# Kernel optimization log

Hardware: AMD Instinct MI355X
Metric: run time of the kernel (lower is better)

Reference implementation:

```python
import jax, jax.numpy as jnp
import numpy as np
from math import sqrt

B, N, D = 16, 4096, 128
M = 64 * 24  # mem_size_per_joint * num_joints


def setup_inputs() -> dict:
    key = jax.random.key(0)
    kx, km = jax.random.split(key)
    x = jax.random.normal(kx, (B, N, D), dtype=jnp.float32)
    mem = jax.random.normal(km, (1, D, M), dtype=jnp.float32)  # N(0,1) init as in torch
    return {"x": x, "mem": mem}


def reference(x, mem):
    # x: (B, N, D); mem: (1, D, M)
    d = x.shape[-1]
    w = mem[0]  # (D, M)
    # logits = bmm(m_key (B,M,D), x_ (B,D,N)) / sqrt(D)  -> (B, M, N)
    logits = jnp.einsum('dm,bnd->bmn', w, x) / sqrt(d)
    # softmax over the memory axis (dim=1 in torch layout)
    attn = jax.nn.softmax(logits, axis=1)  # (B, M, N)
    # x_new = bmm(m (B,D,M), attn) -> (B,D,N); output permuted to (B,N,D)
    out = jnp.einsum('dm,bmn->bnd', w, attn)
    return out
```

## Files before the change

### kernel.cpp

```cpp
#include <hip/hip_runtime.h>
#include <math.h>


#define Bdim 16
#define Ndim 4096
#define Ddim 128
#define Mdim 1536
#define NT 64
#define NTHREADS 256
#define NSESS 12
#define SESS_M 128
#define XPAD 136
#define PPAD 136
#define NFRAG 24576

typedef __attribute__((ext_vector_type(8))) _Float16 f16x8;
typedef __attribute__((ext_vector_type(4))) _Float16 f16x4;
typedef __attribute__((ext_vector_type(4))) float    f32x4;

__global__ void jamb_prep(const float* __restrict__ w,
                          _Float16* __restrict__ wt,
                          _Float16* __restrict__ wd) {
    const int tid = blockIdx.x * 256 + threadIdx.x;
    const float SC = 0.08838834764831843f;
    if (tid < NFRAG) {
        const int f    = tid;
        const int lane = f & 63;
        const int fs   = f >> 6;
        const int ks   = fs & 3;
        const int mt   = fs >> 2;
        const int m    = mt * 16 + (lane & 15);
        const int d0   = ks * 32 + (lane >> 4) * 8;
        f16x8 pk;
        #pragma unroll
        for (int j = 0; j < 8; ++j)
            pk[j] = (_Float16)(w[(size_t)(d0 + j) * Mdim + m] * SC);
        *(f16x8*)&wt[(size_t)f * 8] = pk;
    } else {
        const int f    = tid - NFRAG;
        const int lane = f & 63;
        const int fs   = f >> 6;
        const int km   = fs % 48;
        const int dt   = fs / 48;
        const int d    = dt * 16 + (lane & 15);
        const int m0   = km * 32 + (lane >> 4) * 8;
        const float* src = w + (size_t)d * Mdim + m0;
        const float4 v0 = *(const float4*)src;
        const float4 v1 = *(const float4*)(src + 4);
        f16x8 pk;
        pk[0] = (_Float16)v0.x; pk[1] = (_Float16)v0.y;
        pk[2] = (_Float16)v0.z; pk[3] = (_Float16)v0.w;
        pk[4] = (_Float16)v1.x; pk[5] = (_Float16)v1.y;
        pk[6] = (_Float16)v1.z; pk[7] = (_Float16)v1.w;
        *(f16x8*)&wd[(size_t)f * 8] = pk;
    }
}

__global__ __launch_bounds__(NTHREADS, 4)
void jamb_mfma_kernel(const float* __restrict__ x,
                      const _Float16* __restrict__ wt,
                      const _Float16* __restrict__ wd,
                      float* __restrict__ out) {
    __shared__ __align__(16) _Float16 xs[NT * XPAD];
    __shared__ __align__(16) _Float16 Pbuf[NT * PPAD];
    __shared__ float redsum[4][4][16];

    const int t    = threadIdx.x;
    const int w    = t >> 6;
    const int l    = t & 63;
    const int c16  = l & 15;
    const int quad = l >> 4;

    const int blk   = blockIdx.x;
    const int b     = blk >> 6;
    const int nbase = (blk & 63) * NT;

    {
        const float* xb = x + (size_t)(b * Ndim + nbase) * Ddim;
        #pragma unroll
        for (int i = 0; i < 8; ++i) {
            const int f   = t + i * 256;
            const int row = f >> 5;
            const int c4  = (f & 31) * 4;
            const float4 v = *(const float4*)(xb + row * Ddim + c4);
            f16x4 pk;
            pk[0] = (_Float16)v.x; pk[1] = (_Float16)v.y;
            pk[2] = (_Float16)v.z; pk[3] = (_Float16)v.w;
            *(f16x4*)&xs[row * XPAD + c4] = pk;
        }
    }
    __syncthreads();

    const f16x8* WT = (const f16x8*)wt;
    const f16x8* WD = (const f16x8*)wd;

    float sums[4] = {0.f, 0.f, 0.f, 0.f};
    f32x4 c[2][4];
    #pragma unroll
    for (int i = 0; i < 2; ++i)
        #pragma unroll
        for (int nt = 0; nt < 4; ++nt) c[i][nt] = (f32x4){0.f, 0.f, 0.f, 0.f};

    #pragma unroll 1
    for (int q = 0; q < NSESS; ++q) {
        const int mtb = q * 8 + w * 2;

        f32x4 acc[2][4];
        #pragma unroll
        for (int i = 0; i < 2; ++i)
            #pragma unroll
            for (int nt = 0; nt < 4; ++nt) acc[i][nt] = (f32x4){0.f, 0.f, 0.f, 0.f};

        #pragma unroll
        for (int s = 0; s < 4; ++s) {
            const f16x8 fh0 = WT[((mtb + 0) * 4 + s) * 64 + l];
            const f16x8 fh1 = WT[((mtb + 1) * 4 + s) * 64 + l];
            f16x8 bx[4];
            #pragma unroll
            for (int nt = 0; nt < 4; ++nt)
                bx[nt] = *(const f16x8*)&xs[(nt * 16 + c16) * XPAD + s * 32 + quad * 8];
            #pragma unroll
            for (int nt = 0; nt < 4; ++nt) {
                acc[0][nt] = __builtin_amdgcn_mfma_f32_16x16x32_f16(fh0, bx[nt], acc[0][nt], 0, 0, 0);
                acc[1][nt] = __builtin_amdgcn_mfma_f32_16x16x32_f16(fh1, bx[nt], acc[1][nt], 0, 0, 0);
            }
        }

        #pragma unroll
        for (int i = 0; i < 2; ++i) {
            const int mloc = (w * 2 + i) * 16 + quad * 4;
            #pragma unroll
            for (int nt = 0; nt < 4; ++nt) {
                const float e0 = __expf(acc[i][nt][0]);
                const float e1 = __expf(acc[i][nt][1]);
                const float e2 = __expf(acc[i][nt][2]);
                const float e3 = __expf(acc[i][nt][3]);
                sums[nt] += (e0 + e1) + (e2 + e3);
                f16x4 pk;
                pk[0] = (_Float16)e0; pk[1] = (_Float16)e1;
                pk[2] = (_Float16)e2; pk[3] = (_Float16)e3;
                *(f16x4*)&Pbuf[(nt * 16 + c16) * PPAD + mloc] = pk;
            }
        }
        __syncthreads();

        #pragma unroll
        for (int sk = 0; sk < 4; ++sk) {
            const f16x8 a0 = WD[((2 * w)     * 48 + q * 4 + sk) * 64 + l];
            const f16x8 a1 = WD[((2 * w + 1) * 48 + q * 4 + sk) * 64 + l];
            f16x8 p[4];
            #pragma unroll
            for (int nt = 0; nt < 4; ++nt)
                p[nt] = *(const f16x8*)&Pbuf[(nt * 16 + c16) * PPAD + sk * 32 + quad * 8];
            #pragma unroll
            for (int nt = 0; nt < 4; ++nt) {
                c[0][nt] = __builtin_amdgcn_mfma_f32_16x16x32_f16(a0, p[nt], c[0][nt], 0, 0, 0);
                c[1][nt] = __builtin_amdgcn_mfma_f32_16x16x32_f16(a1, p[nt], c[1][nt], 0, 0, 0);
            }
        }
        __syncthreads();
    }

    #pragma unroll
    for (int nt = 0; nt < 4; ++nt) {
        sums[nt] += __shfl_xor(sums[nt], 16, 64);
        sums[nt] += __shfl_xor(sums[nt], 32, 64);
    }
    if (quad == 0) {
        #pragma unroll
        for (int nt = 0; nt < 4; ++nt) redsum[w][nt][c16] = sums[nt];
    }
    __syncthreads();

    float inv[4];
    #pragma unroll
    for (int nt = 0; nt < 4; ++nt)
        inv[nt] = 1.f / ((redsum[0][nt][c16] + redsum[1][nt][c16]) +
                         (redsum[2][nt][c16] + redsum[3][nt][c16]));

    #pragma unroll
    for (int dt2 = 0; dt2 < 2; ++dt2) {
        #pragma unroll
        for (int nt = 0; nt < 4; ++nt) {
            float* op = out + (size_t)(b * Ndim + nbase + nt * 16 + c16) * Ddim
                           + (2 * w + dt2) * 16 + quad * 4;
            float4 o;
            o.x = c[dt2][nt][0] * inv[nt];
            o.y = c[dt2][nt][1] * inv[nt];
            o.z = c[dt2][nt][2] * inv[nt];
            o.w = c[dt2][nt][3] * inv[nt];
            *(float4*)op = o;
        }
    }
}

extern "C" void kernel_launch(void* const* d_in, const int* in_sizes, int n_in,
                              void* d_out, int out_size, void* d_ws, size_t ws_size,
                              hipStream_t stream) {
    const float* x = (const float*)d_in[0];
    const float* w = (const float*)d_in[1];
    float* out = (float*)d_out;
    (void)in_sizes; (void)n_in; (void)out_size; (void)ws_size;

    _Float16* wt = (_Float16*)d_ws;
    _Float16* wd = wt + Ddim * Mdim;

    jamb_prep<<<dim3((2 * NFRAG) / 256), dim3(256), 0, stream>>>(w, wt, wd);
    jamb_mfma_kernel<<<dim3((Bdim * Ndim) / NT), dim3(NTHREADS), 0, stream>>>(x, wt, wd, out);
}
```

Baseline: 132.6 us.

## Double-buffer softmax tile and overlap logits with output MFMA in smaller sessions

```diff
diff --git a/kernel.cpp b/kernel.cpp
--- a/kernel.cpp
+++ b/kernel.cpp
@@ -8,10 +8,10 @@
 #define Mdim 1536
 #define NT 64
 #define NTHREADS 256
-#define NSESS 12
-#define SESS_M 128
+#define NSESS 24
+#define SESS_M 64
 #define XPAD 136
-#define PPAD 136
+#define PPAD 72
 #define NFRAG 24576
 
 typedef __attribute__((ext_vector_type(8))) _Float16 f16x8;
@@ -22,7 +22,7 @@
                           _Float16* __restrict__ wt,
                           _Float16* __restrict__ wd) {
     const int tid = blockIdx.x * 256 + threadIdx.x;
-    const float SC = 0.08838834764831843f;
+    const float SC = 0.12751742957f;
     if (tid < NFRAG) {
         const int f    = tid;
         const int lane = f & 63;
@@ -62,7 +62,7 @@
                       const _Float16* __restrict__ wd,
                       float* __restrict__ out) {
     __shared__ __align__(16) _Float16 xs[NT * XPAD];
-    __shared__ __align__(16) _Float16 Pbuf[NT * PPAD];
+    __shared__ __align__(16) _Float16 Pbuf[2][NT * PPAD];
     __shared__ float redsum[4][4][16];
 
     const int t    = threadIdx.x;
@@ -101,65 +101,74 @@
         #pragma unroll
         for (int nt = 0; nt < 4; ++nt) c[i][nt] = (f32x4){0.f, 0.f, 0.f, 0.f};
 
-    #pragma unroll 1
-    for (int q = 0; q < NSESS; ++q) {
-        const int mtb = q * 8 + w * 2;
-
-        f32x4 acc[2][4];
-        #pragma unroll
-        for (int i = 0; i < 2; ++i)
-            #pragma unroll
-            for (int nt = 0; nt < 4; ++nt) acc[i][nt] = (f32x4){0.f, 0.f, 0.f, 0.f};
-
+    f16x8 fh[4];
+
+    auto p1load = [&](int sess) {
+        const int mt = sess * 4 + w;
+        #pragma unroll
+        for (int s = 0; s < 4; ++s)
+            fh[s] = WT[(mt * 4 + s) * 64 + l];
+    };
+
+    auto p1 = [&](int sess) {
+        f32x4 acc[4];
+        #pragma unroll
+        for (int nt = 0; nt < 4; ++nt) acc[nt] = (f32x4){0.f, 0.f, 0.f, 0.f};
         #pragma unroll
         for (int s = 0; s < 4; ++s) {
-            const f16x8 fh0 = WT[((mtb + 0) * 4 + s) * 64 + l];
-            const f16x8 fh1 = WT[((mtb + 1) * 4 + s) * 64 + l];
             f16x8 bx[4];
             #pragma unroll
             for (int nt = 0; nt < 4; ++nt)
                 bx[nt] = *(const f16x8*)&xs[(nt * 16 + c16) * XPAD + s * 32 + quad * 8];
             #pragma unroll
-            for (int nt = 0; nt < 4; ++nt) {
-                acc[0][nt] = __builtin_amdgcn_mfma_f32_16x16x32_f16(fh0, bx[nt], acc[0][nt], 0, 0, 0);
-                acc[1][nt] = __builtin_amdgcn_mfma_f32_16x16x32_f16(fh1, bx[nt], acc[1][nt], 0, 0, 0);
-            }
-        }
-
-        #pragma unroll
-        for (int i = 0; i < 2; ++i) {
-            const int mloc = (w * 2 + i) * 16 + quad * 4;
-            #pragma unroll
-            for (int nt = 0; nt < 4; ++nt) {
-                const float e0 = __expf(acc[i][nt][0]);
-                const float e1 = __expf(acc[i][nt][1]);
-                const float e2 = __expf(acc[i][nt][2]);
-                const float e3 = __expf(acc[i][nt][3]);
-                sums[nt] += (e0 + e1) + (e2 + e3);
-                f16x4 pk;
-                pk[0] = (_Float16)e0; pk[1] = (_Float16)e1;
-                pk[2] = (_Float16)e2; pk[3] = (_Float16)e3;
-                *(f16x4*)&Pbuf[(nt * 16 + c16) * PPAD + mloc] = pk;
-            }
-        }
-        __syncthreads();
-
-        #pragma unroll
-        for (int sk = 0; sk < 4; ++sk) {
-            const f16x8 a0 = WD[((2 * w)     * 48 + q * 4 + sk) * 64 + l];
-            const f16x8 a1 = WD[((2 * w + 1) * 48 + q * 4 + sk) * 64 + l];
+            for (int nt = 0; nt < 4; ++nt)
+                acc[nt] = __builtin_amdgcn_mfma_f32_16x16x32_f16(fh[s], bx[nt], acc[nt], 0, 0, 0);
+        }
+        _Float16* Pw = &Pbuf[sess & 1][0];
+        const int mloc = w * 16 + quad * 4;
+        #pragma unroll
+        for (int nt = 0; nt < 4; ++nt) {
+            const float e0 = exp2f(acc[nt][0]);
+            const float e1 = exp2f(acc[nt][1]);
+            const float e2 = exp2f(acc[nt][2]);
+            const float e3 = exp2f(acc[nt][3]);
+            sums[nt] += (e0 + e1) + (e2 + e3);
+            f16x4 pk;
+            pk[0] = (_Float16)e0; pk[1] = (_Float16)e1;
+            pk[2] = (_Float16)e2; pk[3] = (_Float16)e3;
+            *(f16x4*)&Pw[(nt * 16 + c16) * PPAD + mloc] = pk;
+        }
+    };
+
+    auto p2 = [&](int q) {
+        const _Float16* Pr = &Pbuf[q & 1][0];
+        #pragma unroll
+        for (int sk = 0; sk < 2; ++sk) {
+            const f16x8 a0 = WD[((2 * w)     * 48 + q * 2 + sk) * 64 + l];
+            const f16x8 a1 = WD[((2 * w + 1) * 48 + q * 2 + sk) * 64 + l];
             f16x8 p[4];
             #pragma unroll
             for (int nt = 0; nt < 4; ++nt)
-                p[nt] = *(const f16x8*)&Pbuf[(nt * 16 + c16) * PPAD + sk * 32 + quad * 8];
+                p[nt] = *(const f16x8*)&Pr[(nt * 16 + c16) * PPAD + sk * 32 + quad * 8];
             #pragma unroll
             for (int nt = 0; nt < 4; ++nt) {
                 c[0][nt] = __builtin_amdgcn_mfma_f32_16x16x32_f16(a0, p[nt], c[0][nt], 0, 0, 0);
                 c[1][nt] = __builtin_amdgcn_mfma_f32_16x16x32_f16(a1, p[nt], c[1][nt], 0, 0, 0);
             }
         }
+    };
+
+    p1load(0);
+    p1(0);
+    #pragma unroll 1
+    for (int q = 0; q < NSESS - 1; ++q) {
         __syncthreads();
-    }
+        p1load(q + 1);
+        p2(q);
+        p1(q + 1);
+    }
+    __syncthreads();
+    p2(NSESS - 1);
 
     #pragma unroll
     for (int nt = 0; nt < 4; ++nt) {
```

After: 144.0 us. 1.09x slower.
